# Kernel optimization log

Hardware: AMD Instinct MI355X
Metric: run time of the kernel (lower is better)

Reference implementation:

```python
import jax, jax.numpy as jnp
import numpy as np

LX, LY, D, PHYS = 8, 4, 4, 2
NN_ETA = 1e-3


def setup_inputs() -> dict:
    key = jax.random.key(0)
    ks = jax.random.split(key, 6)
    cfg = jax.random.randint(ks[0], (128, LX * LY), 0, 2)
    # PEPS site tensors [Lx, Ly, l, r, d, u, phys]; scaled small so the
    # Lx-long transfer-matrix product stays numerically moderate.
    A = 0.2 * jax.random.normal(ks[1], (LX, LY, D, D, D, D, PHYS), dtype=jnp.float32)
    W1 = jax.random.normal(ks[2], (LX * LY, 64), dtype=jnp.float32) * 0.1
    b1 = jax.random.normal(ks[3], (64,), dtype=jnp.float32) * 0.1
    W2 = jax.random.normal(ks[4], (64, 2 * LX * D * D * D * D * D), dtype=jnp.float32) * 0.05
    b2 = jax.random.normal(ks[5], (2 * LX * D * D * D * D * D,), dtype=jnp.float32) * 0.05
    return {"cfg": cfg, "A": A, "W1": W1, "b1": b1, "W2": W2, "b2": b2}


def reference(cfg, A, W1, b1, W2, b2):
    # A with phys axis moved up front of bond axes for gather: [Lx,Ly,phys,l,r,d,u]
    Ap = jnp.moveaxis(A, -1, 2)
    nb = LX * D * D * D * D * D  # flattened size of one (bottom or top) 2-row half

    def amp(c_flat):
        c = c_flat.reshape(LX, LY)
        # select physical index per site -> [Lx, Ly, l, r, d, u]
        s = jnp.take_along_axis(Ap, c[:, :, None, None, None, None, None], axis=2)[:, :, 0]
        # boundary contraction from ymin: merge rows 0,1 (bottom d-bond projected to 0)
        row0 = s[:, 0, :, :, 0, :]          # [Lx, l, r, u]
        row1 = s[:, 1]                       # [Lx, l, r, d, u]
        bot = jnp.einsum('xlru,xLRuU->xlLrRU', row0, row1).reshape(LX, D * D, D * D, D)
        # boundary contraction from ymax: merge rows 3,2 (top u-bond projected to 0)
        row3 = s[:, 3, :, :, :, 0]           # [Lx, l, r, d]
        row2 = s[:, 2]                       # [Lx, l, r, d, u]
        top = jnp.einsum('xlrdu,xLRu->xlLrRd', row2, row3).reshape(LX, D * D, D * D, D)
        # pack 2-row params into a vector, add MLP correction, unpack
        vec = jnp.concatenate([bot.reshape(-1), top.reshape(-1)])
        h = jax.nn.relu(c_flat.astype(jnp.float32) @ W1 + b1)
        vec = vec + NN_ETA * (h @ W2 + b2)
        bot2 = vec[:nb].reshape(LX, D * D, D * D, D)
        top2 = vec[nb:].reshape(LX, D * D, D * D, D)
        # column transfer matrices and open-boundary chain contraction
        M = jnp.einsum('xiju,xIJu->xiIjJ', bot2, top2).reshape(LX, D ** 4, D ** 4)
        v0 = jnp.zeros(D ** 4, dtype=vec.dtype).at[0].set(1.0)
        def step(v, m):
            return v @ m, None
        v, _ = jax.lax.scan(step, v0, M)
        return v[0]

    return jax.vmap(amp)(cfg)
```

## Files before the change

### kernel.cpp

```cpp
#include <hip/hip_runtime.h>

#define ETA 0.001f
#define NVEC 16384
#define NB   8192

__global__ __launch_bounds__(256) void nn_delta_kernel(
    const int* __restrict__ cfg, const float* __restrict__ W1,
    const float* __restrict__ b1, const float* __restrict__ W2,
    const float* __restrict__ b2, float* __restrict__ delta)
{
    __shared__ float Hs[8][64];
    const int t  = threadIdx.x;
    const int b0 = blockIdx.y * 8;
    const int n4 = blockIdx.x * 256 + t;

    for (int e = t; e < 8 * 64; e += 256) {
        const int bb = e >> 6, k = e & 63;
        float acc = b1[k];
        const int* c = cfg + (b0 + bb) * 32;
        #pragma unroll
        for (int m = 0; m < 32; ++m)
            acc = fmaf((float)c[m], W1[m * 64 + k], acc);
        Hs[bb][k] = fmaxf(acc, 0.0f);
    }
    __syncthreads();

    float4 acc[8];
    #pragma unroll
    for (int bb = 0; bb < 8; ++bb) acc[bb] = make_float4(0.f, 0.f, 0.f, 0.f);

    const float4* W24 = (const float4*)W2;
    #pragma unroll 4
    for (int k = 0; k < 64; ++k) {
        const float4 w = W24[k * 4096 + n4];
        #pragma unroll
        for (int bb = 0; bb < 8; ++bb) {
            const float h = Hs[bb][k];
            acc[bb].x = fmaf(h, w.x, acc[bb].x);
            acc[bb].y = fmaf(h, w.y, acc[bb].y);
            acc[bb].z = fmaf(h, w.z, acc[bb].z);
            acc[bb].w = fmaf(h, w.w, acc[bb].w);
        }
    }
    const float4 bias = ((const float4*)b2)[n4];
    float4* d4 = (float4*)delta;
    #pragma unroll
    for (int bb = 0; bb < 8; ++bb) {
        float4 r;
        r.x = ETA * (acc[bb].x + bias.x);
        r.y = ETA * (acc[bb].y + bias.y);
        r.z = ETA * (acc[bb].z + bias.z);
        r.w = ETA * (acc[bb].w + bias.w);
        d4[(b0 + bb) * 4096 + n4] = r;
    }
}

__global__ __launch_bounds__(256) void contract_kernel(
    const int* __restrict__ cfg, const float* __restrict__ A,
    const float* __restrict__ delta, float* __restrict__ out)
{
    __shared__ float  s[8192];
    __shared__ float  vec[NVEC];
    __shared__ float4 T[256];
    __shared__ float  VT[256];

    const int t = threadIdx.x;
    const int b = blockIdx.x;

    float4 dreg[16];
    const float4* dlt = (const float4*)(delta + b * NVEC);
    #pragma unroll
    for (int q = 0; q < 16; ++q) dreg[q] = dlt[q * 256 + t];

    const int* cb = cfg + b * 32;
    for (int idx = t; idx < 8192; idx += 256)
        s[idx] = A[idx * 2 + cb[idx >> 8]];
    __syncthreads();

    #pragma unroll
    for (int q = 0; q < 16; ++q) {
        const int m = q * 256 + t;
        const int x = (m >> 8) & 7;
        const int i = (m >> 4) & 15;
        const int j = m & 15;
        const int l = i >> 2, L = i & 3, r = j >> 2, R = j & 3;

        float4 acc = make_float4(0.f, 0.f, 0.f, 0.f);
        if (q < 8) {
            const float* sA = s + (x * 4 + 0) * 256;
            const float* sB = sA + 256;
            const float4 a4 = *(const float4*)(sA + l * 64 + r * 16);
            #pragma unroll
            for (int u = 0; u < 4; ++u) {
                const float  a  = (u == 0) ? a4.x : (u == 1) ? a4.y : (u == 2) ? a4.z : a4.w;
                const float4 bv = *(const float4*)(sB + L * 64 + R * 16 + u * 4);
                acc.x = fmaf(a, bv.x, acc.x);
                acc.y = fmaf(a, bv.y, acc.y);
                acc.z = fmaf(a, bv.z, acc.z);
                acc.w = fmaf(a, bv.w, acc.w);
            }
        } else {
            const float* sA = s + (x * 4 + 2) * 256;
            const float* sB = sA + 256;
            const int baseB = L * 64 + R * 16;
            const float4 bvs = make_float4(sB[baseB], sB[baseB + 4], sB[baseB + 8], sB[baseB + 12]);
            const int baseA = l * 64 + r * 16;
            const float4 r0 = *(const float4*)(sA + baseA);
            const float4 r1 = *(const float4*)(sA + baseA + 4);
            const float4 r2 = *(const float4*)(sA + baseA + 8);
            const float4 r3 = *(const float4*)(sA + baseA + 12);
            acc.x = fmaf(r0.x, bvs.x, fmaf(r0.y, bvs.y, fmaf(r0.z, bvs.z, r0.w * bvs.w)));
            acc.y = fmaf(r1.x, bvs.x, fmaf(r1.y, bvs.y, fmaf(r1.z, bvs.z, r1.w * bvs.w)));
            acc.z = fmaf(r2.x, bvs.x, fmaf(r2.y, bvs.y, fmaf(r2.z, bvs.z, r2.w * bvs.w)));
            acc.w = fmaf(r3.x, bvs.x, fmaf(r3.y, bvs.y, fmaf(r3.z, bvs.z, r3.w * bvs.w)));
        }
        const float4 d4 = dreg[q];
        acc.x += d4.x; acc.y += d4.y; acc.z += d4.z; acc.w += d4.w;
        ((float4*)vec)[m] = acc;
    }


    VT[t] = 0.0f;
    __syncthreads();
    if (t == 0) VT[0] = 1.0f;
    __syncthreads();

    const float4* bot4 = (const float4*)vec;
    const float4* top4 = (const float4*)(vec + NB);

    for (int x = 0; x < 8; ++x) {
        {
            const int I = t >> 4, j = t & 15;
            float vv[16];
            *(float4*)&vv[0]  = *(const float4*)(VT + I * 16 + 0);
            *(float4*)&vv[4]  = *(const float4*)(VT + I * 16 + 4);
            *(float4*)&vv[8]  = *(const float4*)(VT + I * 16 + 8);
            *(float4*)&vv[12] = *(const float4*)(VT + I * 16 + 12);
            float4 acc = make_float4(0.f, 0.f, 0.f, 0.f);
            #pragma unroll
            for (int i = 0; i < 16; ++i) {
                const float  vi = vv[i];
                const float4 bv = bot4[x * 256 + i * 16 + j];
                acc.x = fmaf(vi, bv.x, acc.x);
                acc.y = fmaf(vi, bv.y, acc.y);
                acc.z = fmaf(vi, bv.z, acc.z);
                acc.w = fmaf(vi, bv.w, acc.w);
            }
            T[t] = acc;
        }
        __syncthreads();
        {
            const int j = t >> 4, J = t & 15;
            float acc = 0.f;
            #pragma unroll
            for (int I = 0; I < 16; ++I) {
                const float4 tv = T[I * 16 + j];
                const float4 pv = top4[x * 256 + I * 16 + J];
                acc = fmaf(tv.x, pv.x, acc);
                acc = fmaf(tv.y, pv.y, acc);
                acc = fmaf(tv.z, pv.z, acc);
                acc = fmaf(tv.w, pv.w, acc);
            }
            VT[J * 16 + j] = acc;
        }
        __syncthreads();
    }

    if (t == 0) out[b] = VT[0];
}

extern "C" void kernel_launch(void* const* d_in, const int* in_sizes, int n_in,
                              void* d_out, int out_size, void* d_ws, size_t ws_size,
                              hipStream_t stream) {
    const int*   cfg = (const int*)  d_in[0];
    const float* A   = (const float*)d_in[1];
    const float* W1  = (const float*)d_in[2];
    const float* b1  = (const float*)d_in[3];
    const float* W2  = (const float*)d_in[4];
    const float* b2  = (const float*)d_in[5];
    float* out   = (float*)d_out;
    float* delta = (float*)d_ws;

    const int ncfg = in_sizes[0] / 32;

    dim3 gA(16, ncfg / 8);
    nn_delta_kernel<<<gA, 256, 0, stream>>>(cfg, W1, b1, W2, b2, delta);
    contract_kernel<<<ncfg, 256, 0, stream>>>(cfg, A, delta, out);
}
```

Baseline: 96.10 us.

## Contract transfer-matrix chain from both ends concurrently with 512-thread blocks

Splits the 8-step sequential chain contraction into two 4-step halves: one half of the threads propagates the left vector forward while the other half propagates a right vector backward, then a dot-product reduction joins them. This halves the length of the serial dependency chain and its barrier count. The block size doubles to 512, shared arrays are padded to a stride of 17 to reduce bank conflicts, and the gather of A is vectorised. In exchange, shared memory use grows and there is an extra reduction at the end.

```diff
diff --git a/kernel.cpp b/kernel.cpp
--- a/kernel.cpp
+++ b/kernel.cpp
@@ -55,50 +55,58 @@
     }
 }
 
-__global__ __launch_bounds__(256) void contract_kernel(
+__global__ __launch_bounds__(512) void contract_kernel(
     const int* __restrict__ cfg, const float* __restrict__ A,
     const float* __restrict__ delta, float* __restrict__ out)
 {
     __shared__ float  s[8192];
-    __shared__ float  vec[NVEC];
-    __shared__ float4 T[256];
+    __shared__ float4 bot4[8 * 272];
+    __shared__ float4 top4[8 * 272];
+    __shared__ float4 T4[256];
+    __shared__ float4 U4[16 * 17];
     __shared__ float  VT[256];
+    __shared__ float  Wv[16 * 20];
+    __shared__ float  red[8];
 
     const int t = threadIdx.x;
     const int b = blockIdx.x;
 
-    float4 dreg[16];
+    const int* cb = cfg + b * 32;
+    const float4* A4 = (const float4*)A;
+    #pragma unroll
+    for (int k = 0; k < 8; ++k) {
+        const int p = k * 512 + t;
+        const float4 w = A4[p];
+        const int c = cb[p >> 7];
+        float2 r;
+        r.x = c ? w.y : w.x;
+        r.y = c ? w.w : w.z;
+        *(float2*)(s + 2 * p) = r;
+    }
+    __syncthreads();
+
     const float4* dlt = (const float4*)(delta + b * NVEC);
     #pragma unroll
-    for (int q = 0; q < 16; ++q) dreg[q] = dlt[q * 256 + t];
-
-    const int* cb = cfg + b * 32;
-    for (int idx = t; idx < 8192; idx += 256)
-        s[idx] = A[idx * 2 + cb[idx >> 8]];
-    __syncthreads();
-
-    #pragma unroll
-    for (int q = 0; q < 16; ++q) {
-        const int m = q * 256 + t;
+    for (int q = 0; q < 8; ++q) {
+        const int m = q * 512 + t;
         const int x = (m >> 8) & 7;
         const int i = (m >> 4) & 15;
         const int j = m & 15;
         const int l = i >> 2, L = i & 3, r = j >> 2, R = j & 3;
 
         float4 acc = make_float4(0.f, 0.f, 0.f, 0.f);
-        if (q < 8) {
+        if (q < 4) {
             const float* sA = s + (x * 4 + 0) * 256;
             const float* sB = sA + 256;
             const float4 a4 = *(const float4*)(sA + l * 64 + r * 16);
-            #pragma unroll
-            for (int u = 0; u < 4; ++u) {
-                const float  a  = (u == 0) ? a4.x : (u == 1) ? a4.y : (u == 2) ? a4.z : a4.w;
-                const float4 bv = *(const float4*)(sB + L * 64 + R * 16 + u * 4);
-                acc.x = fmaf(a, bv.x, acc.x);
-                acc.y = fmaf(a, bv.y, acc.y);
-                acc.z = fmaf(a, bv.z, acc.z);
-                acc.w = fmaf(a, bv.w, acc.w);
-            }
+            const float4 b0 = *(const float4*)(sB + L * 64 + R * 16 + 0);
+            const float4 b1 = *(const float4*)(sB + L * 64 + R * 16 + 4);
+            const float4 b2 = *(const float4*)(sB + L * 64 + R * 16 + 8);
+            const float4 b3 = *(const float4*)(sB + L * 64 + R * 16 + 12);
+            acc.x = fmaf(a4.x, b0.x, fmaf(a4.y, b1.x, fmaf(a4.z, b2.x, a4.w * b3.x)));
+            acc.y = fmaf(a4.x, b0.y, fmaf(a4.y, b1.y, fmaf(a4.z, b2.y, a4.w * b3.y)));
+            acc.z = fmaf(a4.x, b0.z, fmaf(a4.y, b1.z, fmaf(a4.z, b2.z, a4.w * b3.z)));
+            acc.w = fmaf(a4.x, b0.w, fmaf(a4.y, b1.w, fmaf(a4.z, b2.w, a4.w * b3.w)));
         } else {
             const float* sA = s + (x * 4 + 2) * 256;
             const float* sB = sA + 256;
@@ -114,59 +122,101 @@
             acc.z = fmaf(r2.x, bvs.x, fmaf(r2.y, bvs.y, fmaf(r2.z, bvs.z, r2.w * bvs.w)));
             acc.w = fmaf(r3.x, bvs.x, fmaf(r3.y, bvs.y, fmaf(r3.z, bvs.z, r3.w * bvs.w)));
         }
-        const float4 d4 = dreg[q];
+        const float4 d4 = dlt[m];
         acc.x += d4.x; acc.y += d4.y; acc.z += d4.z; acc.w += d4.w;
-        ((float4*)vec)[m] = acc;
-    }
-
-
-    VT[t] = 0.0f;
-    __syncthreads();
-    if (t == 0) VT[0] = 1.0f;
-    __syncthreads();
-
-    const float4* bot4 = (const float4*)vec;
-    const float4* top4 = (const float4*)(vec + NB);
-
-    for (int x = 0; x < 8; ++x) {
-        {
-            const int I = t >> 4, j = t & 15;
+        float4* dst = (q < 4) ? bot4 : top4;
+        dst[x * 272 + i * 17 + j] = acc;
+    }
+
+    if (t < 256) {
+        VT[t] = (t == 0) ? 1.0f : 0.0f;
+    } else {
+        Wv[t - 256] = (t == 256) ? 1.0f : 0.0f;
+        if (t < 320) Wv[t] = 0.0f;
+    }
+    __syncthreads();
+
+    const int  tr   = t & 255;
+    const bool left = (t < 256);
+    const int  IA = tr >> 4, jA = tr & 15;
+
+    for (int step = 0; step < 4; ++step) {
+        if (left) {
+            const float4* bx = bot4 + step * 272;
             float vv[16];
-            *(float4*)&vv[0]  = *(const float4*)(VT + I * 16 + 0);
-            *(float4*)&vv[4]  = *(const float4*)(VT + I * 16 + 4);
-            *(float4*)&vv[8]  = *(const float4*)(VT + I * 16 + 8);
-            *(float4*)&vv[12] = *(const float4*)(VT + I * 16 + 12);
+            *(float4*)&vv[0]  = *(const float4*)(VT + IA * 16 + 0);
+            *(float4*)&vv[4]  = *(const float4*)(VT + IA * 16 + 4);
+            *(float4*)&vv[8]  = *(const float4*)(VT + IA * 16 + 8);
+            *(float4*)&vv[12] = *(const float4*)(VT + IA * 16 + 12);
             float4 acc = make_float4(0.f, 0.f, 0.f, 0.f);
             #pragma unroll
             for (int i = 0; i < 16; ++i) {
-                const float  vi = vv[i];
-                const float4 bv = bot4[x * 256 + i * 16 + j];
-                acc.x = fmaf(vi, bv.x, acc.x);
-                acc.y = fmaf(vi, bv.y, acc.y);
-                acc.z = fmaf(vi, bv.z, acc.z);
-                acc.w = fmaf(vi, bv.w, acc.w);
-            }
-            T[t] = acc;
+                const float4 bv = bx[i * 17 + jA];
+                acc.x = fmaf(vv[i], bv.x, acc.x);
+                acc.y = fmaf(vv[i], bv.y, acc.y);
+                acc.z = fmaf(vv[i], bv.z, acc.z);
+                acc.w = fmaf(vv[i], bv.w, acc.w);
+            }
+            T4[IA * 16 + jA] = acc;
+        } else {
+            const float4* tx = top4 + (7 - step) * 272;
+            float ww[16];
+            *(float4*)&ww[0]  = *(const float4*)(Wv + jA * 20 + 0);
+            *(float4*)&ww[4]  = *(const float4*)(Wv + jA * 20 + 4);
+            *(float4*)&ww[8]  = *(const float4*)(Wv + jA * 20 + 8);
+            *(float4*)&ww[12] = *(const float4*)(Wv + jA * 20 + 12);
+            float4 acc = make_float4(0.f, 0.f, 0.f, 0.f);
+            #pragma unroll
+            for (int J = 0; J < 16; ++J) {
+                const float4 tv = tx[IA * 17 + J];
+                acc.x = fmaf(ww[J], tv.x, acc.x);
+                acc.y = fmaf(ww[J], tv.y, acc.y);
+                acc.z = fmaf(ww[J], tv.z, acc.z);
+                acc.w = fmaf(ww[J], tv.w, acc.w);
+            }
+            U4[IA * 17 + jA] = acc;
         }
         __syncthreads();
-        {
-            const int j = t >> 4, J = t & 15;
+        if (left) {
+            const int jB = tr >> 4, JB = tr & 15;
+            const float4* tx = top4 + step * 272;
             float acc = 0.f;
             #pragma unroll
             for (int I = 0; I < 16; ++I) {
-                const float4 tv = T[I * 16 + j];
-                const float4 pv = top4[x * 256 + I * 16 + J];
+                const float4 tv = T4[I * 16 + jB];
+                const float4 pv = tx[I * 17 + JB];
                 acc = fmaf(tv.x, pv.x, acc);
                 acc = fmaf(tv.y, pv.y, acc);
                 acc = fmaf(tv.z, pv.z, acc);
                 acc = fmaf(tv.w, pv.w, acc);
             }
-            VT[J * 16 + j] = acc;
+            VT[JB * 16 + jB] = acc;
+        } else {
+            const int iB = tr >> 4, IB = tr & 15;
+            const float4* bx = bot4 + (7 - step) * 272;
+            float acc = 0.f;
+            #pragma unroll
+            for (int j = 0; j < 16; ++j) {
+                const float4 bv = bx[iB * 17 + j];
+                const float4 uv = U4[IB * 17 + j];
+                acc = fmaf(bv.x, uv.x, acc);
+                acc = fmaf(bv.y, uv.y, acc);
+                acc = fmaf(bv.z, uv.z, acc);
+                acc = fmaf(bv.w, uv.w, acc);
+            }
+            Wv[iB * 20 + IB] = acc;
         }
         __syncthreads();
     }
 
-    if (t == 0) out[b] = VT[0];
+    if (t < 256) {
+        float p = VT[t] * Wv[(t & 15) * 20 + (t >> 4)];
+        #pragma unroll
+        for (int off = 32; off > 0; off >>= 1) p += __shfl_down(p, off, 64);
+        if ((t & 63) == 0) red[t >> 6] = p;
+    }
+    __syncthreads();
+    if (t == 0) out[b] = red[0] + red[1] + red[2] + red[3];
 }
 
 extern "C" void kernel_launch(void* const* d_in, const int* in_sizes, int n_in,
@@ -185,5 +235,5 @@
 
     dim3 gA(16, ncfg / 8);
     nn_delta_kernel<<<gA, 256, 0, stream>>>(cfg, W1, b1, W2, b2, delta);
-    contract_kernel<<<ncfg, 256, 0, stream>>>(cfg, A, delta, out);
+    contract_kernel<<<ncfg, 512, 0, stream>>>(cfg, A, delta, out);
 }
```

Result: faster. 90.38 us (-5.9%).
